# Kernel optimization log

Measured on AMD Instinct MI355X. Metric: run time of the kernel, lower is better.

The kernel has to match this reference:

```python
import jax, jax.numpy as jnp
import numpy as np

N_NODES = 50000
N_EDGES = 800000
N_GRAPHS = 128


def gcn_conv(x, row, col, W, b, num_nodes):
    # GCNConv: x' = D^-1/2 (A + I) D^-1/2 (x W) + b, with self-loops added.
    h = x @ W  # [N, out]
    # append self-loops
    sl = jnp.arange(num_nodes, dtype=row.dtype)
    r = jnp.concatenate([row, sl])
    c = jnp.concatenate([col, sl])
    deg = jax.ops.segment_sum(jnp.ones_like(r, dtype=h.dtype), r, num_segments=num_nodes)
    dinv = jnp.where(deg > 0, jax.lax.rsqrt(deg), 0.0)
    norm = dinv[r] * dinv[c]  # [E+N]
    msg = h[c] * norm[:, None]  # gather + scale
    out = jax.ops.segment_sum(msg, r, num_segments=num_nodes)
    return out + b


def setup_inputs() -> dict:
    key = jax.random.key(0)
    k = jax.random.split(key, 6)
    x = jax.random.normal(k[0], (N_NODES, 256), dtype=jnp.float32)
    edge_index = jax.random.randint(k[1], (2, N_EDGES), 0, N_NODES, dtype=jnp.int32)
    batch = jnp.sort(jax.random.randint(k[2], (N_NODES,), 0, N_GRAPHS, dtype=jnp.int32))
    W1 = jax.random.normal(k[3], (256, 128), dtype=jnp.float32) * (1.0 / np.sqrt(256))
    b1 = jnp.zeros((128,), dtype=jnp.float32)
    W2 = jax.random.normal(k[4], (128, 32), dtype=jnp.float32) * (1.0 / np.sqrt(128))
    b2 = jnp.zeros((32,), dtype=jnp.float32)
    return {"x": x, "edge_index": edge_index, "batch": batch,
            "W1": W1, "b1": b1, "W2": W2, "b2": b2}


def reference(x, edge_index, batch, W1, b1, W2, b2):
    row, col = edge_index[0], edge_index[1]
    h = gcn_conv(x, row, col, W1, b1, N_NODES)
    h = jax.nn.relu(h)
    # dropout is identity in eval mode (training=False)
    h = gcn_conv(h, row, col, W2, b2, N_NODES)
    # global_mean_pool over batch ids
    sums = jax.ops.segment_sum(h, batch, num_segments=N_GRAPHS)
    cnts = jax.ops.segment_sum(jnp.ones((N_NODES,), dtype=h.dtype), batch, num_segments=N_GRAPHS)
    pooled = sums / jnp.clip(cnts, 1.0)[:, None]  # [G, num_classes]
    return jax.nn.log_softmax(pooled, axis=1)
```

## Files before the change

### kernel.cpp

```cpp
#include <hip/hip_runtime.h>
#include <hip/hip_bf16.h>
#include <math.h>

#define N_NODES 50000
#define N_EDGES 800000
#define N_GRAPHS 128
#define DIM0 256
#define DIM1 128
#define DIM2 32

#define NBUCK 196
#define NEB 98

using f32x4 = __attribute__((ext_vector_type(4))) float;
using s16x8 = __attribute__((ext_vector_type(8))) short;

__device__ inline unsigned bf16pack(float a, float b) {
    __hip_bfloat162 h2 = __float22bfloat162_rn(make_float2(a, b));
    unsigned r;
    __builtin_memcpy(&r, &h2, 4);
    return r;
}
__device__ inline float2 bf16x2(unsigned p) {
    return make_float2(__uint_as_float(p << 16), __uint_as_float(p & 0xffff0000u));
}

__device__ inline int featOf(int p) {
    return 32 * (p >> 5) + ((p >> 1) & 15) + 16 * (p & 1);
}

__global__ __launch_bounds__(256) void k_hist(const int* __restrict__ row, int* __restrict__ hist) {
    __shared__ int h[NBUCK];
    int b = blockIdx.x, t = threadIdx.x;
    if (t < NBUCK) h[t] = 0;
    __syncthreads();
#pragma unroll
    for (int i = 0; i < 8; ++i) {
        int idx = b * 2048 + i * 256 + t;
        if (idx < N_EDGES / 4) {
            int4 r4 = ((const int4*)row)[idx];
            atomicAdd(&h[r4.x >> 8], 1);
            atomicAdd(&h[r4.y >> 8], 1);
            atomicAdd(&h[r4.z >> 8], 1);
            atomicAdd(&h[r4.w >> 8], 1);
        }
    }
    __syncthreads();
    if (t < NBUCK) hist[b * NBUCK + t] = h[t];
}

__global__ __launch_bounds__(256) void k_place(const int* __restrict__ row, const int* __restrict__ col,
                                               const int* __restrict__ hist, uint* __restrict__ bb,
                                               int* __restrict__ bbase, int* __restrict__ btot,
                                               const float* __restrict__ W1, uint* __restrict__ W1b,
                                               const float* __restrict__ W2, uint* __restrict__ W2b,
                                               const int* __restrict__ batch, int* gstart,
                                               float* __restrict__ pooled) {
    __shared__ int cur[NBUCK];
    __shared__ int tot[NBUCK];
    __shared__ int sc[256];
    int blk = blockIdx.x, t = threadIdx.x;
    if (blk >= NEB) {
        if (blk == NEB + 16) {
            for (int i = t; i < N_GRAPHS * DIM2; i += 256) pooled[i] = 0.f;
            return;
        }
        int g = (blk - NEB) * 256 + t;
        {
            int s = g >> 9, tt = (g >> 6) & 7, q = (g >> 4) & 3, n = g & 15;
            int k0 = s * 32 + q * 8;
            int colw = tt * 16 + n;
            uint4 o;
            o.x = bf16pack(W1[(size_t)(k0 + 0) * DIM1 + colw], W1[(size_t)(k0 + 1) * DIM1 + colw]);
            o.y = bf16pack(W1[(size_t)(k0 + 2) * DIM1 + colw], W1[(size_t)(k0 + 3) * DIM1 + colw]);
            o.z = bf16pack(W1[(size_t)(k0 + 4) * DIM1 + colw], W1[(size_t)(k0 + 5) * DIM1 + colw]);
            o.w = bf16pack(W1[(size_t)(k0 + 6) * DIM1 + colw], W1[(size_t)(k0 + 7) * DIM1 + colw]);
            ((uint4*)W1b)[g] = o;
        }
        if (g < 512) {
            int s = g >> 7, tt = (g >> 6) & 1, l = g & 63;
            int n = tt * 16 + (l & 15);
            int kb = s * 32 + (l >> 4) * 8;
            uint4 o;
            o.x = bf16pack(W2[(size_t)featOf(kb + 0) * DIM2 + n], W2[(size_t)featOf(kb + 1) * DIM2 + n]);
            o.y = bf16pack(W2[(size_t)featOf(kb + 2) * DIM2 + n], W2[(size_t)featOf(kb + 3) * DIM2 + n]);
            o.z = bf16pack(W2[(size_t)featOf(kb + 4) * DIM2 + n], W2[(size_t)featOf(kb + 5) * DIM2 + n]);
            o.w = bf16pack(W2[(size_t)featOf(kb + 6) * DIM2 + n], W2[(size_t)featOf(kb + 7) * DIM2 + n]);
            ((uint4*)W2b)[g] = o;
        }
        if (g <= N_GRAPHS) {
            int lo = 0, hi = N_NODES;
            while (lo < hi) { int mid = (lo + hi) >> 1; if (batch[mid] < g) lo = mid + 1; else hi = mid; }
            gstart[g] = lo;
        }
        return;
    }
    int pre = 0, to = 0;
    for (int b2 = 0; b2 < NEB; ++b2) {
        int v = (t < NBUCK) ? hist[b2 * NBUCK + t] : 0;
        to += v;
        if (b2 < blk) pre += v;
    }
    if (t < NBUCK) tot[t] = to;
    sc[t] = (t < NBUCK) ? to : 0;
    __syncthreads();
    for (int off = 1; off < 256; off <<= 1) {
        int x = (t >= off) ? sc[t - off] : 0;
        __syncthreads();
        sc[t] += x;
        __syncthreads();
    }
    if (t < NBUCK) {
        int base = sc[t] - tot[t];
        cur[t] = base + pre;
        if (blk == 0) { bbase[t] = base; btot[t] = tot[t]; }
    }
    __syncthreads();
#pragma unroll
    for (int i = 0; i < 8; ++i) {
        int idx = blk * 2048 + i * 256 + t;
        if (idx < N_EDGES / 4) {
            int4 r4 = ((const int4*)row)[idx];
            int4 c4 = ((const int4*)col)[idx];
            int rs[4] = {r4.x, r4.y, r4.z, r4.w};
            int cs[4] = {c4.x, c4.y, c4.z, c4.w};
#pragma unroll
            for (int j = 0; j < 4; ++j) {
                int pos = atomicAdd(&cur[rs[j] >> 8], 1);
                bb[pos] = ((uint)(rs[j] & 255) << 16) | (uint)cs[j];
            }
        }
    }
}

__global__ __launch_bounds__(256) void k_build(const int* __restrict__ bbase, const int* __restrict__ btot,
                                               const uint* __restrict__ bb,
                                               int* __restrict__ offs, int* __restrict__ cnt,
                                               ushort* __restrict__ csr) {
    __shared__ int c256[256];
    __shared__ int cur256[256];
    __shared__ int wsum[4];
    int b = blockIdx.x, t = threadIdx.x;
    int start = bbase[b];
    int n = btot[b];
    c256[t] = 0;
    __syncthreads();
    for (int i = t; i < n; i += 256) atomicAdd(&c256[bb[start + i] >> 16], 1);
    __syncthreads();
    int w = t >> 6, l = t & 63;
    int v = c256[t];
    int incl = v;
#pragma unroll
    for (int off = 1; off < 64; off <<= 1) {
        int x = __shfl_up(incl, off, 64);
        if (l >= off) incl += x;
    }
    if (l == 63) wsum[w] = incl;
    __syncthreads();
    int woff = 0;
    for (int i = 0; i < w; ++i) woff += wsum[i];
    int excl = incl - v + woff;
    cur256[t] = excl;
    int r = b * 256 + t;
    if (r < N_NODES) { offs[r] = start + excl; cnt[r] = v; }
    __syncthreads();
    for (int i = t; i < n; i += 256) {
        uint e = bb[start + i];
        int pos = atomicAdd(&cur256[e >> 16], 1);
        csr[start + pos] = (ushort)(e & 0xFFFFu);
    }
}

#define G1_BM 128
#define AS_LD 20
__global__ __launch_bounds__(256) void k_gemm1(const float* __restrict__ X, const uint* __restrict__ W1b,
                                               const int* __restrict__ cnt, unsigned* __restrict__ h1u) {
    __shared__ uint w1s[16384];
    __shared__ uint As[G1_BM * AS_LD];
    int t = threadIdx.x;
    int w = t >> 6, lane = t & 63, q = lane >> 4, m16 = lane & 15;
    int rowBase = blockIdx.x * G1_BM;

    {
        const uint4* src = (const uint4*)W1b;
        uint4* dst = (uint4*)w1s;
#pragma unroll
        for (int i = 0; i < 16; ++i) dst[i * 256 + t] = src[i * 256 + t];
    }

    f32x4 acc[2][8];
#pragma unroll
    for (int i = 0; i < 2; ++i)
#pragma unroll
        for (int j = 0; j < 8; ++j) acc[i][j] = (f32x4){0.f, 0.f, 0.f, 0.f};

    int ar = t >> 1, ah = t & 1;
    for (int s = 0; s < 8; ++s) {
        float4 f0 = {0,0,0,0}, f1 = {0,0,0,0}, f2 = {0,0,0,0}, f3 = {0,0,0,0};
        int grow = rowBase + ar;
        if (grow < N_NODES) {
            const float* src = X + (size_t)grow * DIM0 + s * 32 + ah * 16;
            f0 = *(const float4*)(src + 0);
            f1 = *(const float4*)(src + 4);
            f2 = *(const float4*)(src + 8);
            f3 = *(const float4*)(src + 12);
        }
        uint4 p0, p1;
        p0.x = bf16pack(f0.x, f0.y); p0.y = bf16pack(f0.z, f0.w);
        p0.z = bf16pack(f1.x, f1.y); p0.w = bf16pack(f1.z, f1.w);
        p1.x = bf16pack(f2.x, f2.y); p1.y = bf16pack(f2.z, f2.w);
        p1.z = bf16pack(f3.x, f3.y); p1.w = bf16pack(f3.z, f3.w);
        __syncthreads();
        *(uint4*)&As[ar * AS_LD + ah * 8 + 0] = p0;
        *(uint4*)&As[ar * AS_LD + ah * 8 + 4] = p1;
        __syncthreads();

        s16x8 af[2];
#pragma unroll
        for (int rt = 0; rt < 2; ++rt) {
            int arow = w * 32 + rt * 16 + m16;
            af[rt] = *(s16x8*)&As[arow * AS_LD + q * 4];
        }
#pragma unroll
        for (int tt = 0; tt < 8; ++tt) {
            s16x8 bf = *(s16x8*)&w1s[((s * 8 + tt) * 64 + lane) * 4];
            acc[0][tt] = __builtin_amdgcn_mfma_f32_16x16x32_bf16(af[0], bf, acc[0][tt], 0, 0, 0);
            acc[1][tt] = __builtin_amdgcn_mfma_f32_16x16x32_bf16(af[1], bf, acc[1][tt], 0, 0, 0);
        }
    }

#pragma unroll
    for (int rt = 0; rt < 2; ++rt) {
#pragma unroll
        for (int reg = 0; reg < 4; ++reg) {
            int row = rowBase + w * 32 + rt * 16 + q * 4 + reg;
            if (row < N_NODES) {
                float dv = rsqrtf((float)(cnt[row] + 1));
                unsigned* hr = h1u + (size_t)row * 64;
#pragma unroll
                for (int u = 0; u < 4; ++u)
                    hr[u * 16 + m16] = bf16pack(acc[rt][2 * u][reg] * dv, acc[rt][2 * u + 1][reg] * dv);
            }
        }
    }
}

#define A1_LD 68
__global__ __launch_bounds__(512, 2) void k_agg1g2(const unsigned* __restrict__ h1u, const int* __restrict__ cnt,
                                                   const int* __restrict__ offs, const ushort* __restrict__ csr,
                                                   const float* __restrict__ b1, const uint* __restrict__ W2b,
                                                   unsigned* __restrict__ h2u) {
    __shared__ uint a1tile[16 * A1_LD];
    __shared__ float sdi[16];
    int t = threadIdx.x;
    int wv = t >> 6, lane = t & 63;
    int grp = lane >> 4, li = lane & 15, sub = grp & 1;
    int nb16 = blockIdx.x * 16;
    int mA = wv * 2, mB = wv * 2 + 1;
    int nodeA = nb16 + mA, nodeB = nb16 + mB;
    int nA = cnt[nodeA], nB = cnt[nodeB];
    const ushort* cpA = csr + offs[nodeA];
    const ushort* cpB = csr + offs[nodeB];
    int ecA = (lane < nA) ? (int)cpA[lane] : 0;
    int ecB = (lane < nB) ? (int)cpB[lane] : 0;
    bool isA = grp < 2;
    int nSel = isA ? nA : nB;
    const char* hb = (const char*)h1u;

    float acc[8];
#pragma unroll
    for (int u = 0; u < 8; ++u) acc[u] = 0.f;

    auto accum = [&](uint4 v) {
        float2 a0 = bf16x2(v.x), a1 = bf16x2(v.y), a2 = bf16x2(v.z), a3 = bf16x2(v.w);
        acc[0] += a0.x; acc[1] += a0.y; acc[2] += a1.x; acc[3] += a1.y;
        acc[4] += a2.x; acc[5] += a2.y; acc[6] += a3.x; acc[7] += a3.y;
    };
    auto fetch = [&](int k) -> uint4 {
        int item = 2 * k + sub;
        int cA_ = __shfl(ecA, item);
        int cB_ = __shfl(ecB, item);
        int c = isA ? cA_ : cB_;
        uint4 v = make_uint4(0u, 0u, 0u, 0u);
        if (item < nSel) {
            uint off = (uint)c * 256u + (uint)li * 16u;
            v = *(const uint4*)(hb + off);
        }
        return v;
    };

    if (sub == 0) {
        int selfNode = isA ? nodeA : nodeB;
        uint off = (uint)selfNode * 256u + (uint)li * 16u;
        accum(*(const uint4*)(hb + off));
    }

    int KK = (max(nA, nB) + 1) >> 1;
    for (int k = 0; k < KK; k += 4) {
        uint4 v0 = fetch(k);
        uint4 v1 = fetch(k + 1);
        uint4 v2 = fetch(k + 2);
        uint4 v3 = fetch(k + 3);
        accum(v0); accum(v1); accum(v2); accum(v3);
    }

#pragma unroll
    for (int u = 0; u < 8; ++u) acc[u] += __shfl_xor(acc[u], 16);

    float diA = rsqrtf((float)(nA + 1));
    float diB = rsqrtf((float)(nB + 1));
    if (lane == 0) sdi[mA] = diA;
    if (lane == 32) sdi[mB] = diB;
    float di = isA ? diA : diB;
    int m = isA ? mA : mB;

    uint o0, o1, o2, o3;
    {
        int p = li * 4;
        int flo0 = 32 * (p >> 4) + (p & 15);
        float lo, hi;
        lo = fmaxf(acc[0] * di + b1[flo0 + 0], 0.f);  hi = fmaxf(acc[1] * di + b1[flo0 + 16], 0.f);
        o0 = bf16pack(lo, hi);
        lo = fmaxf(acc[2] * di + b1[flo0 + 1], 0.f);  hi = fmaxf(acc[3] * di + b1[flo0 + 17], 0.f);
        o1 = bf16pack(lo, hi);
        lo = fmaxf(acc[4] * di + b1[flo0 + 2], 0.f);  hi = fmaxf(acc[5] * di + b1[flo0 + 18], 0.f);
        o2 = bf16pack(lo, hi);
        lo = fmaxf(acc[6] * di + b1[flo0 + 3], 0.f);  hi = fmaxf(acc[7] * di + b1[flo0 + 19], 0.f);
        o3 = bf16pack(lo, hi);
    }
    if (sub == 0) {
        *(uint4*)&a1tile[m * A1_LD + li * 4] = make_uint4(o0, o1, o2, o3);
    }
    __syncthreads();

    if (wv == 0) {
        int q = lane >> 4, m16 = lane & 15;
        f32x4 accP = (f32x4){0.f, 0.f, 0.f, 0.f};
        f32x4 accQ = (f32x4){0.f, 0.f, 0.f, 0.f};
#pragma unroll
        for (int s = 0; s < 4; ++s) {
            s16x8 af = *(s16x8*)&a1tile[m16 * A1_LD + s * 16 + q * 4];
            s16x8 bf0 = *(const s16x8*)(W2b + (size_t)((s * 2 + 0) * 64 + lane) * 4);
            s16x8 bf1 = *(const s16x8*)(W2b + (size_t)((s * 2 + 1) * 64 + lane) * 4);
            accP = __builtin_amdgcn_mfma_f32_16x16x32_bf16(af, bf0, accP, 0, 0, 0);
            accQ = __builtin_amdgcn_mfma_f32_16x16x32_bf16(af, bf1, accQ, 0, 0, 0);
        }
#pragma unroll
        for (int r = 0; r < 4; ++r) {
            int node = nb16 + q * 4 + r;
            float dv = sdi[q * 4 + r];
            h2u[(size_t)node * 16 + m16] = bf16pack(accP[r] * dv, accQ[r] * dv);
        }
    }
}

__global__ __launch_bounds__(256) void k_agg2pool(const unsigned* __restrict__ h2u, const int* __restrict__ cnt,
                                                  const int* __restrict__ offs, const ushort* __restrict__ csr,
                                                  const int* __restrict__ batch, float* __restrict__ pooled) {
    __shared__ float2 red[16][16];
    int t = threadIdx.x;
    int nb16 = blockIdx.x * 16;
    int node = nb16 + (t >> 4);
    int l = t & 15;
    float2 acc = bf16x2(h2u[(size_t)node * 16 + l]);
    int n = cnt[node];
    const ushort* cp = csr + offs[node];
    for (int base = 0; base < n; base += 16) {
        int m = min(16, n - base);
        int ec = 0;
        if (l < m) ec = cp[base + l];
        int j = 0;
        if (m == 16) {
            int c[16];
#pragma unroll
            for (int u = 0; u < 16; ++u) c[u] = __shfl(ec, u, 16);
            unsigned p[16];
#pragma unroll
            for (int u = 0; u < 16; ++u) p[u] = h2u[(size_t)c[u] * 16 + l];
            float sx = 0.f, sy = 0.f;
#pragma unroll
            for (int u = 0; u < 16; ++u) { float2 v = bf16x2(p[u]); sx += v.x; sy += v.y; }
            acc.x += sx; acc.y += sy;
            j = 16;
        }
        for (; j + 4 <= m; j += 4) {
            int c0 = __shfl(ec, j, 16), c1 = __shfl(ec, j + 1, 16);
            int c2 = __shfl(ec, j + 2, 16), c3 = __shfl(ec, j + 3, 16);
            unsigned p0 = h2u[(size_t)c0 * 16 + l];
            unsigned p1 = h2u[(size_t)c1 * 16 + l];
            unsigned p2 = h2u[(size_t)c2 * 16 + l];
            unsigned p3 = h2u[(size_t)c3 * 16 + l];
            float2 v0 = bf16x2(p0), v1 = bf16x2(p1), v2 = bf16x2(p2), v3 = bf16x2(p3);
            acc.x += v0.x + v1.x + v2.x + v3.x;
            acc.y += v0.y + v1.y + v2.y + v3.y;
        }
        for (; j < m; ++j) {
            int c = __shfl(ec, j, 16);
            float2 v = bf16x2(h2u[(size_t)c * 16 + l]);
            acc.x += v.x; acc.y += v.y;
        }
    }
    float di = rsqrtf((float)(n + 1));
    red[t >> 4][l] = make_float2(acc.x * di, acc.y * di);
    __syncthreads();
    if (t < 16) {
        float2 run = make_float2(0.f, 0.f);
        int gprev = batch[nb16];
        for (int m = 0; m < 16; ++m) {
            int g = batch[nb16 + m];
            if (g != gprev) {
                atomicAdd(&pooled[gprev * DIM2 + t], run.x);
                atomicAdd(&pooled[gprev * DIM2 + t + 16], run.y);
                run = make_float2(0.f, 0.f);
                gprev = g;
            }
            float2 v = red[m][t];
            run.x += v.x; run.y += v.y;
        }
        atomicAdd(&pooled[gprev * DIM2 + t], run.x);
        atomicAdd(&pooled[gprev * DIM2 + t + 16], run.y);
    }
}

__global__ __launch_bounds__(64) void k_final(const float* __restrict__ pooled, const int* __restrict__ gstart,
                                              const float* __restrict__ b2, float* __restrict__ out) {
    int g = blockIdx.x;
    int lane = threadIdx.x;
    float cntf = fmaxf((float)(gstart[g + 1] - gstart[g]), 1.0f);
    float val = 0.f, v = -INFINITY;
    if (lane < DIM2) {
        val = pooled[g * DIM2 + lane] / cntf + b2[lane];
        v = val;
    }
#pragma unroll
    for (int m = 16; m >= 1; m >>= 1) v = fmaxf(v, __shfl_xor(v, m, 32));
    float ex = (lane < DIM2) ? expf(val - v) : 0.f;
#pragma unroll
    for (int m = 16; m >= 1; m >>= 1) ex += __shfl_xor(ex, m, 32);
    if (lane < DIM2) out[g * DIM2 + lane] = val - v - logf(ex);
}

extern "C" void kernel_launch(void* const* d_in, const int* in_sizes, int n_in,
                              void* d_out, int out_size, void* d_ws, size_t ws_size,
                              hipStream_t stream) {
    const float* x     = (const float*)d_in[0];
    const int*   eidx  = (const int*)d_in[1];
    const int*   batch = (const int*)d_in[2];
    const float* W1    = (const float*)d_in[3];
    const float* b1    = (const float*)d_in[4];
    const float* W2    = (const float*)d_in[5];
    const float* b2    = (const float*)d_in[6];
    const int* row = eidx;
    const int* col = eidx + N_EDGES;
    float* out = (float*)d_out;

    char* p = (char*)d_ws;
    int*    cnt    = (int*)p;    p += (size_t)N_NODES * 4;
    int*    offs   = (int*)p;    p += (size_t)N_NODES * 4 + 16;
    int*    gstart = (int*)p;    p += 768;
    uint*   W1b    = (uint*)p;   p += 4096 * 16;
    uint*   W2b    = (uint*)p;   p += 512 * 16;
    int*    hist   = (int*)p;    p += (size_t)NEB * NBUCK * 4 + 32;
    int*    bbase  = (int*)p;    p += 1024;
    int*    btot   = (int*)p;    p += 1024;
    float*  pooled = (float*)p;  p += (size_t)N_GRAPHS * DIM2 * 4;
    uint*   bb     = (uint*)p;   p += (size_t)N_EDGES * 4;
    ushort* csr    = (ushort*)p; p += (size_t)N_EDGES * 2;
    unsigned* h1u  = (unsigned*)p; p += (size_t)N_NODES * 64 * 4;
    unsigned* h2u  = (unsigned*)p; p += (size_t)N_NODES * 16 * 4;

    k_hist<<<NEB, 256, 0, stream>>>(row, hist);
    k_place<<<NEB + 17, 256, 0, stream>>>(row, col, hist, bb, bbase, btot,
                                          W1, W1b, W2, W2b, batch, gstart, pooled);
    k_build<<<NBUCK, 256, 0, stream>>>(bbase, btot, bb, offs, cnt, csr);

    k_gemm1<<<(N_NODES + G1_BM - 1) / G1_BM, 256, 0, stream>>>(x, W1b, cnt, h1u);
    k_agg1g2<<<N_NODES / 16, 512, 0, stream>>>(h1u, cnt, offs, csr, b1, W2b, h2u);
    k_agg2pool<<<N_NODES / 16, 256, 0, stream>>>(h2u, cnt, offs, csr, batch, pooled);
    k_final<<<N_GRAPHS, 64, 0, stream>>>(pooled, gstart, b2, out);
}
```

Baseline: 189.3 us.

## Widen neighbor gathers to 16-byte loads and stage edge indices in LDS

In the layer-1 aggregation, neighbor indices are now staged in shared memory instead of being selected with two shuffles per fetch, and the gather loop is unrolled from 4 to 8 fetches to keep more loads in flight. In the layer-2 aggregation plus pooling kernel, each 16-lane node group now splits into 4 subgroups that each load 16-byte chunks of different neighbors' 64-byte rows, then combine the partial sums with xor shuffles. This replaces 4-byte per-lane gathers with fewer, wider loads. The cost is higher register use and extra LDS traffic, and the self-loop term is now added only by the first subgroup after the reduction.

```diff
diff --git a/kernel.cpp b/kernel.cpp
--- a/kernel.cpp
+++ b/kernel.cpp
@@ -252,6 +252,7 @@
                                                    unsigned* __restrict__ h2u) {
     __shared__ uint a1tile[16 * A1_LD];
     __shared__ float sdi[16];
+    __shared__ ushort eidx_s[8][2][64];
     int t = threadIdx.x;
     int wv = t >> 6, lane = t & 63;
     int grp = lane >> 4, li = lane & 15, sub = grp & 1;
@@ -263,7 +264,10 @@
     const ushort* cpB = csr + offs[nodeB];
     int ecA = (lane < nA) ? (int)cpA[lane] : 0;
     int ecB = (lane < nB) ? (int)cpB[lane] : 0;
+    eidx_s[wv][0][lane] = (ushort)ecA;
+    eidx_s[wv][1][lane] = (ushort)ecB;
     bool isA = grp < 2;
+    int selIdx = grp >> 1;
     int nSel = isA ? nA : nB;
     const char* hb = (const char*)h1u;
 
@@ -278,12 +282,10 @@
     };
     auto fetch = [&](int k) -> uint4 {
         int item = 2 * k + sub;
-        int cA_ = __shfl(ecA, item);
-        int cB_ = __shfl(ecB, item);
-        int c = isA ? cA_ : cB_;
+        uint c = (uint)eidx_s[wv][selIdx][item & 63];
         uint4 v = make_uint4(0u, 0u, 0u, 0u);
         if (item < nSel) {
-            uint off = (uint)c * 256u + (uint)li * 16u;
+            uint off = c * 256u + (uint)li * 16u;
             v = *(const uint4*)(hb + off);
         }
         return v;
@@ -296,12 +298,17 @@
     }
 
     int KK = (max(nA, nB) + 1) >> 1;
-    for (int k = 0; k < KK; k += 4) {
+    for (int k = 0; k < KK; k += 8) {
         uint4 v0 = fetch(k);
         uint4 v1 = fetch(k + 1);
         uint4 v2 = fetch(k + 2);
         uint4 v3 = fetch(k + 3);
+        uint4 v4 = fetch(k + 4);
+        uint4 v5 = fetch(k + 5);
+        uint4 v6 = fetch(k + 6);
+        uint4 v7 = fetch(k + 7);
         accum(v0); accum(v1); accum(v2); accum(v3);
+        accum(v4); accum(v5); accum(v6); accum(v7);
     }
 
 #pragma unroll
@@ -362,46 +369,52 @@
     int nb16 = blockIdx.x * 16;
     int node = nb16 + (t >> 4);
     int l = t & 15;
-    float2 acc = bf16x2(h2u[(size_t)node * 16 + l]);
+    int sg = l >> 2, li = l & 3;
     int n = cnt[node];
     const ushort* cp = csr + offs[node];
+    const char* hb = (const char*)h2u;
+
+    float acc[8];
+#pragma unroll
+    for (int u = 0; u < 8; ++u) acc[u] = 0.f;
+
+    auto accum = [&](uint4 v) {
+        float2 a0 = bf16x2(v.x), a1 = bf16x2(v.y), a2 = bf16x2(v.z), a3 = bf16x2(v.w);
+        acc[0] += a0.x; acc[1] += a0.y; acc[2] += a1.x; acc[3] += a1.y;
+        acc[4] += a2.x; acc[5] += a2.y; acc[6] += a3.x; acc[7] += a3.y;
+    };
+
     for (int base = 0; base < n; base += 16) {
         int m = min(16, n - base);
-        int ec = 0;
-        if (l < m) ec = cp[base + l];
-        int j = 0;
-        if (m == 16) {
-            int c[16];
-#pragma unroll
-            for (int u = 0; u < 16; ++u) c[u] = __shfl(ec, u, 16);
-            unsigned p[16];
-#pragma unroll
-            for (int u = 0; u < 16; ++u) p[u] = h2u[(size_t)c[u] * 16 + l];
-            float sx = 0.f, sy = 0.f;
-#pragma unroll
-            for (int u = 0; u < 16; ++u) { float2 v = bf16x2(p[u]); sx += v.x; sy += v.y; }
-            acc.x += sx; acc.y += sy;
-            j = 16;
-        }
-        for (; j + 4 <= m; j += 4) {
-            int c0 = __shfl(ec, j, 16), c1 = __shfl(ec, j + 1, 16);
-            int c2 = __shfl(ec, j + 2, 16), c3 = __shfl(ec, j + 3, 16);
-            unsigned p0 = h2u[(size_t)c0 * 16 + l];
-            unsigned p1 = h2u[(size_t)c1 * 16 + l];
-            unsigned p2 = h2u[(size_t)c2 * 16 + l];
-            unsigned p3 = h2u[(size_t)c3 * 16 + l];
-            float2 v0 = bf16x2(p0), v1 = bf16x2(p1), v2 = bf16x2(p2), v3 = bf16x2(p3);
-            acc.x += v0.x + v1.x + v2.x + v3.x;
-            acc.y += v0.y + v1.y + v2.y + v3.y;
-        }
-        for (; j < m; ++j) {
-            int c = __shfl(ec, j, 16);
-            float2 v = bf16x2(h2u[(size_t)c * 16 + l]);
-            acc.x += v.x; acc.y += v.y;
-        }
-    }
+        int ec = (l < m) ? (int)cp[base + l] : 0;
+        uint4 v0 = make_uint4(0u,0u,0u,0u), v1 = v0, v2 = v0, v3 = v0;
+        int i0 = 0 + sg, i1 = 4 + sg, i2 = 8 + sg, i3 = 12 + sg;
+        uint c0 = (uint)__shfl(ec, i0, 16);
+        uint c1 = (uint)__shfl(ec, i1, 16);
+        uint c2 = (uint)__shfl(ec, i2, 16);
+        uint c3 = (uint)__shfl(ec, i3, 16);
+        if (i0 < m) v0 = *(const uint4*)(hb + c0 * 64u + (uint)li * 16u);
+        if (i1 < m) v1 = *(const uint4*)(hb + c1 * 64u + (uint)li * 16u);
+        if (i2 < m) v2 = *(const uint4*)(hb + c2 * 64u + (uint)li * 16u);
+        if (i3 < m) v3 = *(const uint4*)(hb + c3 * 64u + (uint)li * 16u);
+        accum(v0); accum(v1); accum(v2); accum(v3);
+    }
+
+#pragma unroll
+    for (int u = 0; u < 8; ++u) {
+        acc[u] += __shfl_xor(acc[u], 4);
+        acc[u] += __shfl_xor(acc[u], 8);
+    }
+
     float di = rsqrtf((float)(n + 1));
-    red[t >> 4][l] = make_float2(acc.x * di, acc.y * di);
+    if (sg == 0) {
+        uint4 sv = *(const uint4*)(hb + (uint)node * 64u + (uint)li * 16u);
+        accum(sv);
+        int mrow = t >> 4;
+#pragma unroll
+        for (int u = 0; u < 4; ++u)
+            red[mrow][li * 4 + u] = make_float2(acc[2 * u] * di, acc[2 * u + 1] * di);
+    }
     __syncthreads();
     if (t < 16) {
         float2 run = make_float2(0.f, 0.f);
```

Measured after the change: 194.2 us. +2.6%, slower.
